# Kernel tuning notes

Measured on AMD Instinct MI355X. Metric: run time of the kernel, lower is better.

The kernel has to match this reference:

```python
import jax, jax.numpy as jnp
import numpy as np

B, S, D, NH, NKV, HD, FF = 2, 2048, 2048, 16, 8, 128, 8192
EPS = 1e-6
ROPE_THETA = 10000.0


def rmsnorm(x, w):
    return x * jax.lax.rsqrt(jnp.mean(x * x, axis=-1, keepdims=True) + EPS) * w


def rotate_half(x):
    h = x.shape[-1] // 2
    return jnp.concatenate([-x[..., h:], x[..., :h]], axis=-1)


def setup_inputs() -> dict:
    key = jax.random.key(0)
    ks = jax.random.split(key, 32)
    sc = 0.02
    inp = {}
    inp['x'] = jax.random.normal(ks[0], (B, S, D), dtype=jnp.float32)
    pos = jnp.arange(S, dtype=jnp.float32)
    inv = 1.0 / (ROPE_THETA ** (jnp.arange(0, HD, 2, dtype=jnp.float32) / HD))
    fr = jnp.outer(pos, inv)
    emb = jnp.concatenate([fr, fr], axis=-1)  # [S, HD]
    inp['cos'] = jnp.broadcast_to(jnp.cos(emb)[None], (B, S, HD)).astype(jnp.float32)
    inp['sin'] = jnp.broadcast_to(jnp.sin(emb)[None], (B, S, HD)).astype(jnp.float32)
    inp['vision_token_mask'] = jax.random.randint(ks[1], (B, S), 0, 2) > 0
    inp['attn_norm_w'] = jnp.ones((D,), jnp.float32)
    inp['ffn_norm_w'] = jnp.ones((D,), jnp.float32)
    shapes = {
        'wq': (D, NH * HD), 'wk': (D, NKV * HD), 'wv': (D, NKV * HD), 'wo': (NH * HD, D),
        'mm_wq': (D, NH * HD), 'mm_wk': (D, NKV * HD), 'mm_wv': (D, NKV * HD), 'mm_wo': (NH * HD, D),
        'gate_w': (D, FF), 'up_w': (D, FF), 'down_w': (FF, D),
        'mm_gate_w': (D, FF), 'mm_up_w': (D, FF), 'mm_down_w': (FF, D),
    }
    for i, (name, shp) in enumerate(shapes.items()):
        inp[name] = jax.random.normal(ks[2 + i], shp, dtype=jnp.float32) * sc
    for name in ['q_norm_w', 'k_norm_w', 'mm_q_norm_w', 'mm_k_norm_w']:
        inp[name] = jnp.ones((HD,), jnp.float32)
    return inp


def gpt_block(x, cos, sin, mask, attn_norm_w, ffn_norm_w,
              wq, wk, wv, wo, mm_wq, mm_wk, mm_wv, mm_wo,
              q_norm_w, k_norm_w, mm_q_norm_w, mm_k_norm_w,
              gate_w, up_w, down_w, mm_gate_w, mm_up_w, mm_down_w):
    m2 = mask[..., None]            # [B,S,1]
    m4 = mask[:, :, None, None]     # [B,S,1,1]
    h = rmsnorm(x, attn_norm_w)
    # dual-path QKV: text tokens use plain weights, vision tokens use mm_* weights
    q_t = rmsnorm((h @ wq).reshape(B, S, NH, HD), q_norm_w)
    q_v = rmsnorm((h @ mm_wq).reshape(B, S, NH, HD), mm_q_norm_w)
    q = jnp.where(m4, q_v, q_t)
    k_t = rmsnorm((h @ wk).reshape(B, S, NKV, HD), k_norm_w)
    k_v = rmsnorm((h @ mm_wk).reshape(B, S, NKV, HD), mm_k_norm_w)
    k = jnp.where(m4, k_v, k_t)
    v = jnp.where(m2, h @ mm_wv, h @ wv).reshape(B, S, NKV, HD)
    # RoPE (unsqueeze over head dim)
    cu = cos[:, :, None, :]
    su = sin[:, :, None, :]
    q = q * cu + rotate_half(q) * su
    k = k * cu + rotate_half(k) * su
    # GQA repeat + causal attention
    rep = NH // NKV
    k_r = jnp.repeat(k, rep, axis=2)
    v_r = jnp.repeat(v, rep, axis=2)
    scale = 1.0 / jnp.sqrt(jnp.float32(HD))
    scores = jnp.einsum('bqhd,bkhd->bhqk', q, k_r) * scale
    causal = jnp.tril(jnp.ones((S, S), bool))
    scores = jnp.where(causal, scores, jnp.float32(-1e30))
    p = jax.nn.softmax(scores, axis=-1)
    attn = jnp.einsum('bhqk,bkhd->bqhd', p, v_r).reshape(B, S, NH * HD)
    attn_out = jnp.where(m2, attn @ mm_wo, attn @ wo)
    h2 = x + attn_out
    # dual-path SwiGLU FFN
    g = rmsnorm(h2, ffn_norm_w)
    ff_t = (jax.nn.silu(g @ gate_w) * (g @ up_w)) @ down_w
    ff_v = (jax.nn.silu(g @ mm_gate_w) * (g @ mm_up_w)) @ mm_down_w
    return h2 + jnp.where(m2, ff_v, ff_t)


def reference(x, cos, sin, vision_token_mask, attn_norm_w, ffn_norm_w,
              wq, wk, wv, wo, mm_wq, mm_wk, mm_wv, mm_wo,
              q_norm_w, k_norm_w, mm_q_norm_w, mm_k_norm_w,
              gate_w, up_w, down_w, mm_gate_w, mm_up_w, mm_down_w):
    return gpt_block(x, cos, sin, vision_token_mask, attn_norm_w, ffn_norm_w,
                     wq, wk, wv, wo, mm_wq, mm_wk, mm_wv, mm_wo,
                     q_norm_w, k_norm_w, mm_q_norm_w, mm_k_norm_w,
                     gate_w, up_w, down_w, mm_gate_w, mm_up_w, mm_down_w)
```

## Files before the change

kernel.cpp:

```cpp
#include <hip/hip_runtime.h>

typedef unsigned short u16;
typedef __bf16 bf16x8 __attribute__((ext_vector_type(8)));
typedef float f32x4 __attribute__((ext_vector_type(4)));

__device__ __forceinline__ u16 f2bf(float f) {
    unsigned u = __builtin_bit_cast(unsigned, f);
    u += 0x7fffu + ((u >> 16) & 1u);
    return (u16)(u >> 16);
}
__device__ __forceinline__ float bf2f(u16 v) {
    unsigned u = ((unsigned)v) << 16;
    return __builtin_bit_cast(float, u);
}
__device__ __forceinline__ void glds16(const void* g, void* l) {
    __builtin_amdgcn_global_load_lds(
        (const __attribute__((address_space(1))) unsigned*)g,
        (__attribute__((address_space(3))) unsigned*)l, 16, 0, 0);
}

__device__ __forceinline__ void xcd_map(int bid, int nloc, int TM, int& tm, int& tn)
{
    const int xcd = bid & 7;
    int l = bid >> 3;
    const int per = nloc << 3;
    const int fullC = TM >> 3;
    const int lFull = fullC * per;
    int c, tn_l, tmIn;
    if (l < lFull) { c = l / per; int r = l - c * per; tn_l = r >> 3; tmIn = r & 7; }
    else { int r = l - lFull; int sc = TM - (fullC << 3); c = fullC; tn_l = r / sc; tmIn = r % sc; }
    tm = (c << 3) + tmIn;
    tn = xcd * nloc + tn_l;
}

__device__ __forceinline__ void swz_src(int r, int sp, int& rs, int& ks)
{
    int e = (((r & 1) << 2) | sp) ^ ((r >> 1) & 7);
    rs = (r & ~1) | (e >> 2);
    ks = e & 3;
}
__device__ __forceinline__ int swz_rd(int row, int lg)
{
    int s8 = (((row & 1) << 2) | lg) ^ ((row >> 1) & 7);
    return (row >> 1) * 128 + s8 * 16;
}

__global__ __launch_bounds__(1024) void build_perm(
    const int* __restrict__ mask, int* __restrict__ perm, int* __restrict__ counts)
{
    __shared__ int sc[1024];
    int t = threadIdx.x;
    int m[4], cnt = 0;
#pragma unroll
    for (int j = 0; j < 4; j++) {
        m[j] = mask[t * 4 + j] != 0;
        cnt += (m[j] == 0);
    }
    sc[t] = cnt;
    __syncthreads();
    for (int off = 1; off < 1024; off <<= 1) {
        int v = (t >= off) ? sc[t - off] : 0;
        __syncthreads();
        sc[t] += v;
        __syncthreads();
    }
    int totT = sc[1023];
    int exT = sc[t] - cnt;
    int exV = t * 4 - exT;
    int pT = exT, pV = totT + exV;
#pragma unroll
    for (int j = 0; j < 4; j++) {
        if (m[j] == 0) perm[pT++] = t * 4 + j;
        else           perm[pV++] = t * 4 + j;
    }
    if (t == 0) { counts[0] = totT; counts[1] = 4096 - totT; }
}

__global__ __launch_bounds__(256) void transpose_bf16(
    const float* __restrict__ W, u16* __restrict__ Wt, int Kd, int Nd)
{
    __shared__ float tile[64][65];
    int k0 = blockIdx.x * 64, n0 = blockIdx.y * 64;
    int t = threadIdx.x;
    int rr = t >> 4, cc = (t & 15) * 4;
#pragma unroll
    for (int i = 0; i < 4; i++) {
        float4 v = *(const float4*)&W[(long)(k0 + i * 16 + rr) * Nd + n0 + cc];
        tile[i * 16 + rr][cc]     = v.x;
        tile[i * 16 + rr][cc + 1] = v.y;
        tile[i * 16 + rr][cc + 2] = v.z;
        tile[i * 16 + rr][cc + 3] = v.w;
    }
    __syncthreads();
    int nn = t >> 3, k8 = (t & 7) * 8;
#pragma unroll
    for (int i = 0; i < 2; i++) {
        int n = i * 32 + nn;
        u16 pk[8];
#pragma unroll
        for (int j = 0; j < 8; j++) pk[j] = f2bf(tile[k8 + j][n]);
        *(uint4*)&Wt[(long)(n0 + n) * Kd + k0 + k8] = *(const uint4*)pk;
    }
}

__global__ __launch_bounds__(256) void rms_x(
    const float* __restrict__ x, const float* __restrict__ w, u16* __restrict__ out)
{
    long row = blockIdx.x;
    int t = threadIdx.x, wave = t >> 6, lane = t & 63;
    const float4* x4 = (const float4*)(x + row * 2048);
    float4 a = x4[2 * t], b = x4[2 * t + 1];
    float ss = a.x*a.x + a.y*a.y + a.z*a.z + a.w*a.w
             + b.x*b.x + b.y*b.y + b.z*b.z + b.w*b.w;
#pragma unroll
    for (int m = 1; m < 64; m <<= 1) ss += __shfl_xor(ss, m);
    __shared__ float red[4];
    if (lane == 0) red[wave] = ss;
    __syncthreads();
    float tot = red[0] + red[1] + red[2] + red[3];
    float inv = rsqrtf(tot * (1.0f / 2048.0f) + 1e-6f);
    const float4* w4 = (const float4*)w;
    float4 wa = w4[2 * t], wb = w4[2 * t + 1];
    u16* op = out + row * 2048 + t * 8;
    op[0] = f2bf(a.x * inv * wa.x); op[1] = f2bf(a.y * inv * wa.y);
    op[2] = f2bf(a.z * inv * wa.z); op[3] = f2bf(a.w * inv * wa.w);
    op[4] = f2bf(b.x * inv * wb.x); op[5] = f2bf(b.y * inv * wb.y);
    op[6] = f2bf(b.z * inv * wb.z); op[7] = f2bf(b.w * inv * wb.w);
}

template <int EPI, bool PG, bool PC>
__global__ __launch_bounds__(512, 4) void gemm32(
    const u16* __restrict__ A, const u16* __restrict__ Bt0, const u16* __restrict__ Bt1,
    void* __restrict__ Cv,
    const int* __restrict__ perm, const int* __restrict__ counts, int N, int K)
{
    extern __shared__ u16 lds[];
    int tm, tn;
    xcd_map(blockIdx.x, N >> 11, 33, tm, tn);
    const int nT = counts[0];
    const int tT = (nT + 127) >> 7, tV = (4096 - nT + 127) >> 7;
    if (tm >= tT + tV) return;
    const bool vis = tm >= tT;
    const u16* Bt = vis ? Bt1 : Bt0;
    const int rowbase = vis ? nT + (tm - tT) * 128 : tm * 128;
    const int rowlim = vis ? 4096 : nT;
    const int tid = threadIdx.x;
    const int wave = tid >> 6, lane = tid & 63;
    const int wrbase = (wave >> 2) * 64, wcbase = (wave & 3) * 64;
    const int lr = lane & 15, lg = lane >> 4;
    const int n0 = tn * 256;
    const int t4 = tid >> 2, sp = tid & 3;
    const char* aSrc;
    const char* bSrc[2];
    {
        int rs, ks; swz_src(t4, sp, rs, ks);
        int gr = rowbase + rs; gr = gr < 4095 ? gr : 4095;
        long ar = PG ? perm[gr] : gr;
        aSrc = (const char*)A + ar * (long)K * 2 + ks * 16;
    }
#pragma unroll
    for (int c = 0; c < 2; c++) {
        int r = c * 128 + t4;
        int rs, ks; swz_src(r, sp, rs, ks);
        bSrc[c] = (const char*)Bt + (long)(n0 + rs) * K * 2 + ks * 16;
    }
    auto stage = [&](int kt, int bu) {
        char* ab = (char*)lds + bu * 24576;
        long ko = (long)kt * 64;
        glds16(aSrc + ko, ab + tid * 16);
#pragma unroll
        for (int c = 0; c < 2; c++)
            glds16(bSrc[c] + ko, ab + 8192 + c * 8192 + tid * 16);
    };
    auto ldA = [&](int bu, int mi) -> bf16x8 {
        const char* ab = (const char*)lds + bu * 24576;
        int row = wrbase + mi * 16 + lr;
        return *(const bf16x8*)(ab + swz_rd(row, lg));
    };
    auto ldB = [&](int bu, int ni) -> bf16x8 {
        const char* bb = (const char*)lds + bu * 24576 + 8192;
        int row = wcbase + ni * 16 + lr;
        return *(const bf16x8*)(bb + swz_rd(row, lg));
    };

    f32x4 acc[4][4] = {};
    const int nkt = K >> 5;
    stage(0, 0);
    stage(1, 1);
    for (int kt = 0; kt < nkt; ++kt) {
        const int bu = kt % 3;
        if (kt == nkt - 1) asm volatile("s_waitcnt vmcnt(0)" ::: "memory");
        else               asm volatile("s_waitcnt vmcnt(3)" ::: "memory");
        __builtin_amdgcn_s_barrier();
        if (kt + 2 < nkt) stage(kt + 2, (kt + 2) % 3);
        bf16x8 af[4], bq[4];
#pragma unroll
        for (int i = 0; i < 4; i++) af[i] = ldA(bu, i);
#pragma unroll
        for (int j = 0; j < 4; j++) bq[j] = ldB(bu, j);
        __builtin_amdgcn_s_setprio(1);
#pragma unroll
        for (int i = 0; i < 4; i++)
#pragma unroll
            for (int j = 0; j < 4; j++)
                acc[i][j] = __builtin_amdgcn_mfma_f32_16x16x32_bf16(
                    af[i], bq[j], acc[i][j], 0, 0, 0);
        __builtin_amdgcn_s_setprio(0);
    }
#pragma unroll
    for (int mi = 0; mi < 4; mi++)
#pragma unroll
        for (int r = 0; r < 4; r++) {
            int gr = rowbase + wrbase + mi * 16 + lg * 4 + r;
            if (gr >= rowlim) continue;
            long crow = PC ? (long)perm[gr] : (long)gr;
#pragma unroll
            for (int ni = 0; ni < 4; ni++) {
                long col = n0 + wcbase + ni * 16 + lr;
                ((u16*)Cv)[crow * (long)N + col] = f2bf(acc[mi][ni][r]);
            }
        }
}

__global__ __launch_bounds__(512, 4) void gemm_gu(
    const u16* __restrict__ A,
    const u16* __restrict__ Bg0, const u16* __restrict__ Bg1,
    const u16* __restrict__ Bu0, const u16* __restrict__ Bu1,
    u16* __restrict__ C,
    const int* __restrict__ perm, const int* __restrict__ counts, int N, int K)
{
    extern __shared__ u16 lds[];
    int tm, tn;
    xcd_map(blockIdx.x, N >> 10, 33, tm, tn);
    const int nT = counts[0];
    const int tT = (nT + 127) >> 7, tV = (4096 - nT + 127) >> 7;
    if (tm >= tT + tV) return;
    const bool vis = tm >= tT;
    const u16* Bg = vis ? Bg1 : Bg0;
    const u16* Bu = vis ? Bu1 : Bu0;
    const int rowbase = vis ? nT + (tm - tT) * 128 : tm * 128;
    const int rowlim = vis ? 4096 : nT;
    const int tid = threadIdx.x;
    const int wave = tid >> 6, lane = tid & 63;
    const int wrbase = (wave >> 2) * 64, wcbase = (wave & 3) * 32;
    const int lr = lane & 15, lg = lane >> 4;
    const int n0 = tn * 128;
    const int t4 = tid >> 2, sp = tid & 3;
    const char *aSrc, *gSrc, *uSrc;
    {
        int rs, ks; swz_src(t4, sp, rs, ks);
        int gr = rowbase + rs; gr = gr < 4095 ? gr : 4095;
        long ar = (long)perm[gr];
        aSrc = (const char*)A + ar * (long)K * 2 + ks * 16;
        gSrc = (const char*)Bg + (long)(n0 + rs) * K * 2 + ks * 16;
        uSrc = (const char*)Bu + (long)(n0 + rs) * K * 2 + ks * 16;
    }
    auto stage = [&](int kt, int bu) {
        char* ab = (char*)lds + bu * 24576;
        long ko = (long)kt * 64;
        glds16(aSrc + ko, ab + tid * 16);
        glds16(gSrc + ko, ab + 8192 + tid * 16);
        glds16(uSrc + ko, ab + 16384 + tid * 16);
    };
    auto ldA = [&](int bu, int mi) -> bf16x8 {
        const char* ab = (const char*)lds + bu * 24576;
        int row = wrbase + mi * 16 + lr;
        return *(const bf16x8*)(ab + swz_rd(row, lg));
    };
    auto ldGU = [&](int bu, int sub, int ni) -> bf16x8 {
        const char* p = (const char*)lds + bu * 24576 + 8192 + sub * 8192;
        int row = wcbase + ni * 16 + lr;
        return *(const bf16x8*)(p + swz_rd(row, lg));
    };

    f32x4 accg[4][2] = {}, accu[4][2] = {};
    const int nkt = K >> 5;
    stage(0, 0);
    stage(1, 1);
    for (int kt = 0; kt < nkt; ++kt) {
        const int bu = kt % 3;
        if (kt == nkt - 1) asm volatile("s_waitcnt vmcnt(0)" ::: "memory");
        else               asm volatile("s_waitcnt vmcnt(3)" ::: "memory");
        __builtin_amdgcn_s_barrier();
        if (kt + 2 < nkt) stage(kt + 2, (kt + 2) % 3);
        bf16x8 af[4], bg[2], bv[2];
#pragma unroll
        for (int i = 0; i < 4; i++) af[i] = ldA(bu, i);
#pragma unroll
        for (int j = 0; j < 2; j++) {
            bg[j] = ldGU(bu, 0, j);
            bv[j] = ldGU(bu, 1, j);
        }
        __builtin_amdgcn_s_setprio(1);
#pragma unroll
        for (int i = 0; i < 4; i++)
#pragma unroll
            for (int j = 0; j < 2; j++) {
                accg[i][j] = __builtin_amdgcn_mfma_f32_16x16x32_bf16(
                    af[i], bg[j], accg[i][j], 0, 0, 0);
                accu[i][j] = __builtin_amdgcn_mfma_f32_16x16x32_bf16(
                    af[i], bv[j], accu[i][j], 0, 0, 0);
            }
        __builtin_amdgcn_s_setprio(0);
    }
#pragma unroll
    for (int mi = 0; mi < 4; mi++)
#pragma unroll
        for (int r = 0; r < 4; r++) {
            int gr = rowbase + wrbase + mi * 16 + lg * 4 + r;
            if (gr >= rowlim) continue;
#pragma unroll
            for (int ni = 0; ni < 2; ni++) {
                long col = n0 + wcbase + ni * 16 + lr;
                float g = accg[mi][ni][r], u = accu[mi][ni][r];
                C[(long)gr * N + col] = f2bf(g / (1.0f + __expf(-g)) * u);
            }
        }
}

template <int EPI, bool PG, bool PC>
__global__ __launch_bounds__(512, 4) void gemmsq(
    const u16* __restrict__ A, const u16* __restrict__ Bt0, const u16* __restrict__ Bt1,
    void* __restrict__ Cv, const float* __restrict__ resid,
    const int* __restrict__ perm, const int* __restrict__ counts, int N, int K)
{
    extern __shared__ u16 lds[];
    int tm, tn;
    xcd_map(blockIdx.x, N >> 10, 33, tm, tn);
    const int nT = counts[0];
    const int tT = (nT + 127) >> 7, tV = (4096 - nT + 127) >> 7;
    if (tm >= tT + tV) return;
    const bool vis = tm >= tT;
    const u16* Bt = vis ? Bt1 : Bt0;
    const int rowbase = vis ? nT + (tm - tT) * 128 : tm * 128;
    const int rowlim = vis ? 4096 : nT;
    const int tid = threadIdx.x;
    const int wave = tid >> 6, lane = tid & 63;
    const int wrbase = (wave >> 2) * 64, wcbase = (wave & 3) * 32;
    const int lr = lane & 15, lg = lane >> 4;
    const int n0 = tn * 128;
    const int t4 = tid >> 2, sp = tid & 3;
    const char *aSrc, *bSrc;
    {
        int rs, ks; swz_src(t4, sp, rs, ks);
        int gr = rowbase + rs; gr = gr < 4095 ? gr : 4095;
        long ar = PG ? (long)perm[gr] : (long)gr;
        aSrc = (const char*)A + ar * (long)K * 2 + ks * 16;
        bSrc = (const char*)Bt + (long)(n0 + rs) * K * 2 + ks * 16;
    }
    auto stage = [&](int kt, int bu) {
        char* ab = (char*)lds + bu * 16384;
        long ko = (long)kt * 64;
        glds16(aSrc + ko, ab + tid * 16);
        glds16(bSrc + ko, ab + 8192 + tid * 16);
    };
    auto ldA = [&](int bu, int mi) -> bf16x8 {
        const char* ab = (const char*)lds + bu * 16384;
        int row = wrbase + mi * 16 + lr;
        return *(const bf16x8*)(ab + swz_rd(row, lg));
    };
    auto ldB = [&](int bu, int ni) -> bf16x8 {
        const char* bb = (const char*)lds + bu * 16384 + 8192;
        int row = wcbase + ni * 16 + lr;
        return *(const bf16x8*)(bb + swz_rd(row, lg));
    };

    f32x4 acc[4][2] = {};
    const int nkt = K >> 5;
    stage(0, 0);
    for (int kt = 0; kt < nkt; ++kt) {
        const int bu = kt & 1;
        __syncthreads();
        if (kt + 1 < nkt) stage(kt + 1, bu ^ 1);
        bf16x8 af[4], bq[2];
#pragma unroll
        for (int i = 0; i < 4; i++) af[i] = ldA(bu, i);
#pragma unroll
        for (int j = 0; j < 2; j++) bq[j] = ldB(bu, j);
        __builtin_amdgcn_s_setprio(1);
#pragma unroll
        for (int i = 0; i < 4; i++)
#pragma unroll
            for (int j = 0; j < 2; j++)
                acc[i][j] = __builtin_amdgcn_mfma_f32_16x16x32_bf16(
                    af[i], bq[j], acc[i][j], 0, 0, 0);
        __builtin_amdgcn_s_setprio(0);
    }
#pragma unroll
    for (int mi = 0; mi < 4; mi++)
#pragma unroll
        for (int r = 0; r < 4; r++) {
            int gr = rowbase + wrbase + mi * 16 + lg * 4 + r;
            if (gr >= rowlim) continue;
            long crow = PC ? (long)perm[gr] : (long)gr;
#pragma unroll
            for (int ni = 0; ni < 2; ni++) {
                long col = n0 + wcbase + ni * 16 + lr;
                long idx = crow * (long)N + col;
                ((float*)Cv)[idx] = resid[idx] + acc[mi][ni][r];
            }
        }
}

template <int EPI, bool PG, bool PC>
__global__ __launch_bounds__(512, 2) void gemmk(
    const u16* __restrict__ A, const u16* __restrict__ Bt0, const u16* __restrict__ Bt1,
    void* __restrict__ Cv, const float* __restrict__ resid,
    const int* __restrict__ perm, const int* __restrict__ counts, int N, int K)
{
    extern __shared__ u16 lds[];
    int tm, tn;
    xcd_map(blockIdx.x, N >> 11, 33, tm, tn);
    const int nT = counts[0];
    const int tT = (nT + 127) >> 7, tV = (4096 - nT + 127) >> 7;
    if (tm >= tT + tV) return;
    const bool vis = tm >= tT;
    const u16* Bt = vis ? Bt1 : Bt0;
    const int rowbase = vis ? nT + (tm - tT) * 128 : tm * 128;
    const int rowlim = vis ? 4096 : nT;
    const int tid = threadIdx.x;
    const int wave = tid >> 6, lane = tid & 63;
    const int wrbase = (wave >> 2) * 64, wcbase = (wave & 3) * 64;
    const int lr = lane & 15, lg = lane >> 4;
    const int n0 = tn * 256;
    const int t8 = tid >> 3, sp = tid & 7;
    const char* aSrc[2];
    const char* bSrc[4];
#pragma unroll
    for (int c = 0; c < 2; c++) {
        int r = c * 64 + t8;
        int gr = rowbase + r; gr = gr < 4095 ? gr : 4095;
        long ar = PG ? perm[gr] : gr;
        aSrc[c] = (const char*)A + ar * (long)K * 2 + ((sp ^ (r & 7)) << 4);
    }
#pragma unroll
    for (int c = 0; c < 4; c++) {
        int r = c * 64 + t8;
        bSrc[c] = (const char*)Bt + (long)(n0 + r) * K * 2 + ((sp ^ (r & 7)) << 4);
    }
    auto stage = [&](int kt, int bu) {
        char* ab = (char*)lds + bu * 49152;
        char* bb = ab + 16384;
        long ko = (long)kt * 128;
#pragma unroll
        for (int c = 0; c < 2; c++)
            glds16(aSrc[c] + ko, ab + c * 8192 + tid * 16);
#pragma unroll
        for (int c = 0; c < 4; c++)
            glds16(bSrc[c] + ko, bb + c * 8192 + tid * 16);
    };
    auto ldA = [&](int bu, int mi, int kk) -> bf16x8 {
        const char* ab = (const char*)lds + bu * 49152;
        int row = wrbase + mi * 16 + lr;
        int sl = kk * 4 + lg;
        return *(const bf16x8*)(ab + row * 128 + ((sl ^ (row & 7)) << 4));
    };
    auto ldB = [&](int bu, int ni, int kk) -> bf16x8 {
        const char* bb = (const char*)lds + bu * 49152 + 16384;
        int row = wcbase + ni * 16 + lr;
        int sl = kk * 4 + lg;
        return *(const bf16x8*)(bb + row * 128 + ((sl ^ (row & 7)) << 4));
    };

    f32x4 acc[4][4] = {};
    const int nkt = K >> 6;
    stage(0, 0);
    stage(1, 1);
    for (int kt = 0; kt < nkt; ++kt) {
        const int bu = kt % 3;
        if (kt == nkt - 1) asm volatile("s_waitcnt vmcnt(0)" ::: "memory");
        else               asm volatile("s_waitcnt vmcnt(6)" ::: "memory");
        __builtin_amdgcn_s_barrier();
        if (kt + 2 < nkt) stage(kt + 2, (kt + 2) % 3);
#pragma unroll
        for (int kk = 0; kk < 2; kk++) {
            bf16x8 af[4], bq[4];
#pragma unroll
            for (int i = 0; i < 4; i++) af[i] = ldA(bu, i, kk);
#pragma unroll
            for (int j = 0; j < 4; j++) bq[j] = ldB(bu, j, kk);
            __builtin_amdgcn_s_setprio(1);
#pragma unroll
            for (int i = 0; i < 4; i++)
#pragma unroll
                for (int j = 0; j < 4; j++)
                    acc[i][j] = __builtin_amdgcn_mfma_f32_16x16x32_bf16(
                        af[i], bq[j], acc[i][j], 0, 0, 0);
            __builtin_amdgcn_s_setprio(0);
        }
    }
#pragma unroll
    for (int mi = 0; mi < 4; mi++)
#pragma unroll
        for (int r = 0; r < 4; r++) {
            int gr = rowbase + wrbase + mi * 16 + lg * 4 + r;
            if (gr >= rowlim) continue;
            long crow = PC ? (long)perm[gr] : (long)gr;
#pragma unroll
            for (int ni = 0; ni < 4; ni++) {
                long col = n0 + wcbase + ni * 16 + lr;
                long idx = crow * (long)N + col;
                float v = acc[mi][ni][r];
                if (EPI == 1)      ((u16*)Cv)[idx] = f2bf(v);
                else if (EPI == 2) ((float*)Cv)[idx] = resid[idx] + v;
            }
        }
}

__global__ __launch_bounds__(256) void qk_fuse(
    const u16* __restrict__ p, const int* __restrict__ mask,
    const float* __restrict__ cs, const float* __restrict__ sn,
    const float* __restrict__ nwt, const float* __restrict__ nwv,
    u16* __restrict__ out, int H, int stride)
{
    int wave = threadIdx.x >> 6, lane = threadIdx.x & 63;
    int gw = blockIdx.x * 4 + wave;
    int tok = gw / H, h = gw % H;
    int b = tok >> 11, s = tok & 2047;
    const u16* src = p + (long)tok * stride + h * 128;
    const float* w = mask[tok] ? nwv : nwt;
    int d = lane * 2;
    float yx = bf2f(src[d]), yy = bf2f(src[d + 1]);
    float ss = yx * yx + yy * yy;
#pragma unroll
    for (int m = 1; m < 64; m <<= 1) ss += __shfl_xor(ss, m);
    float inv = rsqrtf(ss * (1.0f / 128.0f) + 1e-6f);
    float y0 = yx * inv * w[d], y1 = yy * inv * w[d + 1];
    float o0 = __shfl_xor(y0, 32), o1 = __shfl_xor(y1, 32);
    float sgn = (lane < 32) ? -1.0f : 1.0f;
    const float* cp = cs + (long)tok * 128 + d;
    const float* spn = sn + (long)tok * 128 + d;
    float r0 = y0 * cp[0] + sgn * o0 * spn[0];
    float r1 = y1 * cp[1] + sgn * o1 * spn[1];
    u16* op = out + (((long)b * H + h) * 2048 + s) * 128 + d;
    op[0] = f2bf(r0); op[1] = f2bf(r1);
}

__global__ __launch_bounds__(256) void v_fuse(
    const u16* __restrict__ vsrc, u16* __restrict__ outv, int stride)
{
    __shared__ u16 tile[32][33];
    int s0 = blockIdx.x * 32, d0 = blockIdx.y * 32;
    int bkv = blockIdx.z, b = bkv >> 3, kv = bkv & 7;
    int tx = threadIdx.x, ty = threadIdx.y;
#pragma unroll
    for (int i = 0; i < 32; i += 8) {
        long tok = (long)b * 2048 + s0 + ty + i;
        tile[ty + i][tx] = vsrc[tok * stride + kv * 128 + d0 + tx];
    }
    __syncthreads();
#pragma unroll
    for (int i = 0; i < 32; i += 8)
        outv[(((long)b * 8 + kv) * 128 + d0 + ty + i) * 2048 + s0 + tx] =
            tile[tx][ty + i];
}

__global__ __launch_bounds__(256) void attn_fwd(
    const u16* __restrict__ q, const u16* __restrict__ k,
    const u16* __restrict__ v, u16* __restrict__ out)
{
    __shared__ u16 Ks[32 * 128];
    __shared__ u16 Vs[128 * 32];
    __shared__ u16 Ps[4][16][40];
    const int tid = threadIdx.x, wave = tid >> 6, lane = tid & 63;
    const int lr = lane & 15, lg = lane >> 4;
    const int b = blockIdx.z, h = blockIdx.y, q0 = blockIdx.x * 64;
    const int kvh = h >> 1;
    const u16* qp = q + (((long)b * 16 + h) * 2048 + q0 + wave * 16) * 128;
    bf16x8 qf[4];
#pragma unroll
    for (int f = 0; f < 4; f++)
        qf[f] = *(const bf16x8*)(qp + (long)lr * 128 + f * 32 + lg * 8);
    const char* kbase = (const char*)(k + ((long)b * 8 + kvh) * 2048 * 128);
    const char* vbase = (const char*)(v + ((long)b * 8 + kvh) * 128 * 2048);
    f32x4 o[8] = {};
    float lsum[4] = {};
    const float sc2 = 0.08838834764831845f * 1.44269504088896f;
    const float MB = 16.5f;
    const int ntiles = (q0 + 64) >> 5;
    for (int t = 0; t < ntiles; ++t) {
        int kv0 = t * 32;
        __syncthreads();
#pragma unroll
        for (int j = 0; j < 2; j++) {
            int L = (j * 4 + wave) * 1024 + lane * 16;
            {
                int row = L >> 8, cb = L & 255;
                glds16(kbase + (long)(kv0 + row) * 256 + (cb ^ ((row & 7) << 4)),
                       (char*)Ks + (j * 4 + wave) * 1024);
            }
            {
                int row = L >> 6, cb = L & 63;
                glds16(vbase + (long)row * 4096 + kv0 * 2 + (cb ^ ((row & 3) << 4)),
                       (char*)Vs + (j * 4 + wave) * 1024);
            }
        }
        __syncthreads();
        f32x4 s[2] = {};
#pragma unroll
        for (int sub = 0; sub < 2; ++sub)
#pragma unroll
            for (int f = 0; f < 4; ++f) {
                int row = sub * 16 + lr;
                int cb = (f * 64 + lg * 16) ^ ((row & 7) << 4);
                bf16x8 kf = *(const bf16x8*)((const char*)Ks + row * 256 + cb);
                s[sub] = __builtin_amdgcn_mfma_f32_16x16x32_bf16(qf[f], kf, s[sub], 0, 0, 0);
            }
#pragma unroll
        for (int r = 0; r < 4; r++) {
            int rowg = q0 + wave * 16 + lg * 4 + r;
            float s0 = s[0][r] * sc2 - MB; if (kv0 + lr > rowg)      s0 = -1e30f;
            float s1 = s[1][r] * sc2 - MB; if (kv0 + 16 + lr > rowg) s1 = -1e30f;
            float p0 = exp2f(s0), p1 = exp2f(s1);
            lsum[r] += p0 + p1;
            int prow = lg * 4 + r;
            Ps[wave][prow][lr] = f2bf(p0);
            Ps[wave][prow][16 + lr] = f2bf(p1);
        }
        bf16x8 pf = *(const bf16x8*)&Ps[wave][lr][lg * 8];
#pragma unroll
        for (int ni = 0; ni < 8; ni++) {
            int row = ni * 16 + lr;
            int cb = (lg * 16) ^ ((row & 3) << 4);
            bf16x8 vf = *(const bf16x8*)((const char*)Vs + row * 64 + cb);
            o[ni] = __builtin_amdgcn_mfma_f32_16x16x32_bf16(pf, vf, o[ni], 0, 0, 0);
        }
    }
#pragma unroll
    for (int r = 0; r < 4; r++)
#pragma unroll
        for (int mm = 1; mm < 16; mm <<= 1) lsum[r] += __shfl_xor(lsum[r], mm);
#pragma unroll
    for (int ni = 0; ni < 8; ni++)
#pragma unroll
        for (int r = 0; r < 4; r++) {
            long row = (long)b * 2048 + q0 + wave * 16 + lg * 4 + r;
            out[row * 2048 + h * 128 + ni * 16 + lr] = f2bf(o[ni][r] / lsum[r]);
        }
}

extern "C" void kernel_launch(void* const* d_in, const int* in_sizes, int n_in,
                              void* d_out, int out_size, void* d_ws, size_t ws_size,
                              hipStream_t stream)
{
    const float* x    = (const float*)d_in[0];
    const float* cosp = (const float*)d_in[1];
    const float* sinp = (const float*)d_in[2];
    const int*   mask = (const int*)d_in[3];
    const float* anw  = (const float*)d_in[4];
    const float* fnw  = (const float*)d_in[5];
    const float* wq   = (const float*)d_in[6];
    const float* wk   = (const float*)d_in[7];
    const float* wv   = (const float*)d_in[8];
    const float* wo   = (const float*)d_in[9];
    const float* mwq  = (const float*)d_in[10];
    const float* mwk  = (const float*)d_in[11];
    const float* mwv  = (const float*)d_in[12];
    const float* mwo  = (const float*)d_in[13];
    const float* gw   = (const float*)d_in[14];
    const float* uw   = (const float*)d_in[15];
    const float* dw   = (const float*)d_in[16];
    const float* mgw  = (const float*)d_in[17];
    const float* muw  = (const float*)d_in[18];
    const float* mdw  = (const float*)d_in[19];
    const float* qnw  = (const float*)d_in[20];
    const float* knw  = (const float*)d_in[21];
    const float* mqnw = (const float*)d_in[22];
    const float* mknw = (const float*)d_in[23];

    char* base = (char*)d_ws;
    u16* wA0   = (u16*)(base);
    u16* wA1   = (u16*)(base + (32u << 20));
    u16* wB0   = (u16*)(base + (64u << 20));
    u16* wB1   = (u16*)(base + (96u << 20));
    u16* hbf   = (u16*)(base + (64u << 20));
    u16* qkv   = (u16*)(base + (80u << 20));
    u16* qb    = (u16*)(base + (112u << 20));
    u16* kb    = (u16*)(base + (128u << 20));
    u16* vb    = (u16*)(base + (136u << 20));
    u16* attnb = (u16*)(base + (144u << 20));
    u16* e1    = (u16*)(base + (128u << 20));
    float* h2  = (float*)(base + (192u << 20));
    u16* gbf   = (u16*)(base + (224u << 20));
    int* perm  = (int*)(base + (240u << 20));
    int* cnts  = perm + 4096;

    hipFuncSetAttribute((const void*)&gemm32<1, true, true>,
                        hipFuncAttributeMaxDynamicSharedMemorySize, 73728);
    hipFuncSetAttribute((const void*)&gemm_gu,
                        hipFuncAttributeMaxDynamicSharedMemorySize, 73728);
    hipFuncSetAttribute((const void*)&gemmk<2, true, true>,
                        hipFuncAttributeMaxDynamicSharedMemorySize, 147456);

    auto TR = [&](const float* w, u16* dst, int K, int N) {
        transpose_bf16<<<dim3(K / 64, N / 64), 256, 0, stream>>>(w, dst, K, N);
    };

    build_perm<<<1, 1024, 0, stream>>>(mask, perm, cnts);
    rms_x<<<4096, 256, 0, stream>>>(x, anw, hbf);

    TR(wq, wA0, 2048, 2048);
    TR(wk, wA0 + (long)2048 * 2048, 2048, 1024);
    TR(wv, wA0 + (long)3072 * 2048, 2048, 1024);
    TR(mwq, wA1, 2048, 2048);
    TR(mwk, wA1 + (long)2048 * 2048, 2048, 1024);
    TR(mwv, wA1 + (long)3072 * 2048, 2048, 1024);
    gemm32<1, true, true><<<528, 512, 73728, stream>>>(
        hbf, wA0, wA1, (void*)qkv, perm, cnts, 4096, 2048);

    qk_fuse<<<16384, 256, 0, stream>>>(qkv, mask, cosp, sinp, qnw, mqnw, qb, 16, 4096);
    qk_fuse<<<8192, 256, 0, stream>>>(qkv + 2048, mask, cosp, sinp, knw, mknw, kb, 8, 4096);
    v_fuse<<<dim3(64, 4, 16), dim3(32, 8), 0, stream>>>(qkv + 3072, vb, 4096);

    attn_fwd<<<dim3(32, 16, 2), 256, 0, stream>>>(qb, kb, vb, attnb);

    TR(wo, wA0, 2048, 2048); TR(mwo, wA1, 2048, 2048);
    gemmk<2, true, true><<<264, 512, 147456, stream>>>(
        attnb, wA0, wA1, (void*)h2, x, perm, cnts, 2048, 2048);

    rms_x<<<4096, 256, 0, stream>>>(h2, fnw, gbf);

    TR(gw, wA0, 2048, 8192); TR(mgw, wA1, 2048, 8192);
    TR(uw, wB0, 2048, 8192); TR(muw, wB1, 2048, 8192);
    gemm_gu<<<2112, 512, 73728, stream>>>(
        gbf, wA0, wA1, wB0, wB1, e1, perm, cnts, 8192, 2048);
    TR(dw, wA0, 8192, 2048); TR(mdw, wA1, 8192, 2048);
    gemmsq<2, false, true><<<528, 512, 32768, stream>>>(
        e1, wA0, wA1, (void*)d_out, h2, perm, cnts, 2048, 8192);
}
```

Before: 1.028 ms.

## Deepen K-tiles in down-proj GEMM and double-buffer 64-wide KV tiles in attention

```diff
diff --git a/kernel.cpp b/kernel.cpp
--- a/kernel.cpp
+++ b/kernel.cpp
@@ -339,52 +339,61 @@
     const int wrbase = (wave >> 2) * 64, wcbase = (wave & 3) * 32;
     const int lr = lane & 15, lg = lane >> 4;
     const int n0 = tn * 128;
-    const int t4 = tid >> 2, sp = tid & 3;
-    const char *aSrc, *bSrc;
-    {
-        int rs, ks; swz_src(t4, sp, rs, ks);
-        int gr = rowbase + rs; gr = gr < 4095 ? gr : 4095;
+    const int t8 = tid >> 3, sp = tid & 7;
+    const char *aSrc[2], *bSrc[2];
+#pragma unroll
+    for (int c = 0; c < 2; c++) {
+        int r = c * 64 + t8;
+        int gr = rowbase + r; gr = gr < 4095 ? gr : 4095;
         long ar = PG ? (long)perm[gr] : (long)gr;
-        aSrc = (const char*)A + ar * (long)K * 2 + ks * 16;
-        bSrc = (const char*)Bt + (long)(n0 + rs) * K * 2 + ks * 16;
+        aSrc[c] = (const char*)A + ar * (long)K * 2 + ((sp ^ (r & 7)) << 4);
+        bSrc[c] = (const char*)Bt + (long)(n0 + r) * K * 2 + ((sp ^ (r & 7)) << 4);
     }
     auto stage = [&](int kt, int bu) {
-        char* ab = (char*)lds + bu * 16384;
-        long ko = (long)kt * 64;
-        glds16(aSrc + ko, ab + tid * 16);
-        glds16(bSrc + ko, ab + 8192 + tid * 16);
-    };
-    auto ldA = [&](int bu, int mi) -> bf16x8 {
-        const char* ab = (const char*)lds + bu * 16384;
+        char* ab = (char*)lds + bu * 32768;
+        long ko = (long)kt * 128;
+#pragma unroll
+        for (int c = 0; c < 2; c++) {
+            glds16(aSrc[c] + ko, ab + c * 8192 + tid * 16);
+            glds16(bSrc[c] + ko, ab + 16384 + c * 8192 + tid * 16);
+        }
+    };
+    auto ldA = [&](int bu, int mi, int kk) -> bf16x8 {
+        const char* ab = (const char*)lds + bu * 32768;
         int row = wrbase + mi * 16 + lr;
-        return *(const bf16x8*)(ab + swz_rd(row, lg));
-    };
-    auto ldB = [&](int bu, int ni) -> bf16x8 {
-        const char* bb = (const char*)lds + bu * 16384 + 8192;
+        int sl = kk * 4 + lg;
+        return *(const bf16x8*)(ab + row * 128 + ((sl ^ (row & 7)) << 4));
+    };
+    auto ldB = [&](int bu, int ni, int kk) -> bf16x8 {
+        const char* bb = (const char*)lds + bu * 32768 + 16384;
         int row = wcbase + ni * 16 + lr;
-        return *(const bf16x8*)(bb + swz_rd(row, lg));
+        int sl = kk * 4 + lg;
+        return *(const bf16x8*)(bb + row * 128 + ((sl ^ (row & 7)) << 4));
     };
 
     f32x4 acc[4][2] = {};
-    const int nkt = K >> 5;
+    const int nkt = K >> 6;
     stage(0, 0);
     for (int kt = 0; kt < nkt; ++kt) {
         const int bu = kt & 1;
         __syncthreads();
         if (kt + 1 < nkt) stage(kt + 1, bu ^ 1);
-        bf16x8 af[4], bq[2];
-#pragma unroll
-        for (int i = 0; i < 4; i++) af[i] = ldA(bu, i);
-#pragma unroll
-        for (int j = 0; j < 2; j++) bq[j] = ldB(bu, j);
-        __builtin_amdgcn_s_setprio(1);
-#pragma unroll
-        for (int i = 0; i < 4; i++)
-#pragma unroll
-            for (int j = 0; j < 2; j++)
-                acc[i][j] = __builtin_amdgcn_mfma_f32_16x16x32_bf16(
-                    af[i], bq[j], acc[i][j], 0, 0, 0);
-        __builtin_amdgcn_s_setprio(0);
+#pragma unroll
+        for (int kk = 0; kk < 2; kk++) {
+            bf16x8 af[4], bq[2];
+#pragma unroll
+            for (int i = 0; i < 4; i++) af[i] = ldA(bu, i, kk);
+#pragma unroll
+            for (int j = 0; j < 2; j++) bq[j] = ldB(bu, j, kk);
+            __builtin_amdgcn_s_setprio(1);
+#pragma unroll
+            for (int i = 0; i < 4; i++)
+#pragma unroll
+                for (int j = 0; j < 2; j++)
+                    acc[i][j] = __builtin_amdgcn_mfma_f32_16x16x32_bf16(
+                        af[i], bq[j], acc[i][j], 0, 0, 0);
+            __builtin_amdgcn_s_setprio(0);
+        }
     }
 #pragma unroll
     for (int mi = 0; mi < 4; mi++)
@@ -559,9 +568,10 @@
     const u16* __restrict__ q, const u16* __restrict__ k,
     const u16* __restrict__ v, u16* __restrict__ out)
 {
-    __shared__ u16 Ks[32 * 128];
-    __shared__ u16 Vs[128 * 32];
-    __shared__ u16 Ps[4][16][40];
+    extern __shared__ char alds[];
+    char* KsB = alds;
+    char* VsB = alds + 32768;
+    u16* Ps   = (u16*)(alds + 65536);
     const int tid = threadIdx.x, wave = tid >> 6, lane = tid & 63;
     const int lr = lane & 15, lg = lane >> 4;
     const int b = blockIdx.z, h = blockIdx.y, q0 = blockIdx.x * 64;
@@ -577,54 +587,70 @@
     float lsum[4] = {};
     const float sc2 = 0.08838834764831845f * 1.44269504088896f;
     const float MB = 16.5f;
-    const int ntiles = (q0 + 64) >> 5;
-    for (int t = 0; t < ntiles; ++t) {
-        int kv0 = t * 32;
-        __syncthreads();
-#pragma unroll
-        for (int j = 0; j < 2; j++) {
-            int L = (j * 4 + wave) * 1024 + lane * 16;
+    const int ntiles = (q0 >> 6) + 1;
+    auto stageKV = [&](int t, int bu) {
+        char* kd = KsB + bu * 16384;
+        char* vd = VsB + bu * 16384;
+        long kv0 = (long)t * 64;
+#pragma unroll
+        for (int c = 0; c < 4; c++) {
+            int L = c * 4096 + tid * 16;
             {
                 int row = L >> 8, cb = L & 255;
-                glds16(kbase + (long)(kv0 + row) * 256 + (cb ^ ((row & 7) << 4)),
-                       (char*)Ks + (j * 4 + wave) * 1024);
+                glds16(kbase + (kv0 + row) * 256 + (cb ^ ((row & 7) << 4)), kd + L);
             }
             {
-                int row = L >> 6, cb = L & 63;
-                glds16(vbase + (long)row * 4096 + kv0 * 2 + (cb ^ ((row & 3) << 4)),
-                       (char*)Vs + (j * 4 + wave) * 1024);
-            }
-        }
+                int row = L >> 7, cb = L & 127;
+                glds16(vbase + (long)row * 4096 + kv0 * 2 + (cb ^ ((row & 7) << 4)), vd + L);
+            }
+        }
+    };
+    stageKV(0, 0);
+    for (int t = 0; t < ntiles; ++t) {
+        const int bu = t & 1;
         __syncthreads();
-        f32x4 s[2] = {};
-#pragma unroll
-        for (int sub = 0; sub < 2; ++sub)
+        if (t + 1 < ntiles) stageKV(t + 1, bu ^ 1);
+        const char* Ks = KsB + bu * 16384;
+        const char* Vs = VsB + bu * 16384;
+        f32x4 s[4] = {};
+#pragma unroll
+        for (int nf = 0; nf < 4; ++nf)
 #pragma unroll
             for (int f = 0; f < 4; ++f) {
-                int row = sub * 16 + lr;
+                int row = nf * 16 + lr;
                 int cb = (f * 64 + lg * 16) ^ ((row & 7) << 4);
-                bf16x8 kf = *(const bf16x8*)((const char*)Ks + row * 256 + cb);
-                s[sub] = __builtin_amdgcn_mfma_f32_16x16x32_bf16(qf[f], kf, s[sub], 0, 0, 0);
-            }
+                bf16x8 kf = *(const bf16x8*)(Ks + row * 256 + cb);
+                s[nf] = __builtin_amdgcn_mfma_f32_16x16x32_bf16(qf[f], kf, s[nf], 0, 0, 0);
+            }
+        int kv0 = t * 64;
 #pragma unroll
         for (int r = 0; r < 4; r++) {
             int rowg = q0 + wave * 16 + lg * 4 + r;
-            float s0 = s[0][r] * sc2 - MB; if (kv0 + lr > rowg)      s0 = -1e30f;
-            float s1 = s[1][r] * sc2 - MB; if (kv0 + 16 + lr > rowg) s1 = -1e30f;
-            float p0 = exp2f(s0), p1 = exp2f(s1);
-            lsum[r] += p0 + p1;
-            int prow = lg * 4 + r;
-            Ps[wave][prow][lr] = f2bf(p0);
-            Ps[wave][prow][16 + lr] = f2bf(p1);
-        }
-        bf16x8 pf = *(const bf16x8*)&Ps[wave][lr][lg * 8];
-#pragma unroll
-        for (int ni = 0; ni < 8; ni++) {
-            int row = ni * 16 + lr;
-            int cb = (lg * 16) ^ ((row & 3) << 4);
-            bf16x8 vf = *(const bf16x8*)((const char*)Vs + row * 64 + cb);
-            o[ni] = __builtin_amdgcn_mfma_f32_16x16x32_bf16(pf, vf, o[ni], 0, 0, 0);
-        }
+            int prow = (wave * 16 + lg * 4 + r) * 72;
+            float ls = 0.0f;
+#pragma unroll
+            for (int nf = 0; nf < 4; nf++) {
+                float sv = s[nf][r] * sc2 - MB;
+                if (kv0 + nf * 16 + lr > rowg) sv = -1e30f;
+                float p = exp2f(sv);
+                ls += p;
+                Ps[prow + nf * 16 + lr] = f2bf(p);
+            }
+            lsum[r] += ls;
+        }
+        bf16x8 pf[2];
+#pragma unroll
+        for (int kk = 0; kk < 2; kk++)
+            pf[kk] = *(const bf16x8*)&Ps[(wave * 16 + lr) * 72 + kk * 32 + lg * 8];
+#pragma unroll
+        for (int ni = 0; ni < 8; ni++)
+#pragma unroll
+            for (int kk = 0; kk < 2; kk++) {
+                int row = ni * 16 + lr;
+                int cb = (kk * 64 + lg * 16) ^ ((row & 7) << 4);
+                bf16x8 vf = *(const bf16x8*)(Vs + row * 128 + cb);
+                o[ni] = __builtin_amdgcn_mfma_f32_16x16x32_bf16(pf[kk], vf, o[ni], 0, 0, 0);
+            }
     }
 #pragma unroll
     for (int r = 0; r < 4; r++)
@@ -691,6 +717,10 @@
                         hipFuncAttributeMaxDynamicSharedMemorySize, 73728);
     hipFuncSetAttribute((const void*)&gemmk<2, true, true>,
                         hipFuncAttributeMaxDynamicSharedMemorySize, 147456);
+    hipFuncSetAttribute((const void*)&gemmsq<2, false, true>,
+                        hipFuncAttributeMaxDynamicSharedMemorySize, 65536);
+    hipFuncSetAttribute((const void*)&attn_fwd,
+                        hipFuncAttributeMaxDynamicSharedMemorySize, 74752);
 
     auto TR = [&](const float* w, u16* dst, int K, int N) {
         transpose_bf16<<<dim3(K / 64, N / 64), 256, 0, stream>>>(w, dst, K, N);
@@ -712,7 +742,7 @@
     qk_fuse<<<8192, 256, 0, stream>>>(qkv + 2048, mask, cosp, sinp, knw, mknw, kb, 8, 4096);
     v_fuse<<<dim3(64, 4, 16), dim3(32, 8), 0, stream>>>(qkv + 3072, vb, 4096);
 
-    attn_fwd<<<dim3(32, 16, 2), 256, 0, stream>>>(qb, kb, vb, attnb);
+    attn_fwd<<<dim3(32, 16, 2), 256, 74752, stream>>>(qb, kb, vb, attnb);
 
     TR(wo, wA0, 2048, 2048); TR(mwo, wA1, 2048, 2048);
     gemmk<2, true, true><<<264, 512, 147456, stream>>>(
@@ -725,6 +755,6 @@
     gemm_gu<<<2112, 512, 73728, stream>>>(
         gbf, wA0, wA1, wB0, wB1, e1, perm, cnts, 8192, 2048);
     TR(dw, wA0, 8192, 2048); TR(mdw, wA1, 8192, 2048);
-    gemmsq<2, false, true><<<528, 512, 32768, stream>>>(
+    gemmsq<2, false, true><<<528, 512, 65536, stream>>>(
         e1, wA0, wA1, (void*)d_out, h2, perm, cnts, 2048, 8192);
 }
```

Measured after the change: 1.073 ms. +4.4%, slower.
